# Kernel optimization log

Measured on AMD Instinct MI355X. Metric: run time of the kernel, lower is better.

## Reference

```python
import jax, jax.numpy as jnp
import numpy as np

N_HEAD = 16

def setup_inputs() -> dict:
    key = jax.random.key(0)
    ks = jax.random.split(key, 9)
    H = 2048
    def w(k, shape, scale=0.02):
        return jax.random.normal(k, shape, dtype=jnp.float32) * scale
    return {
        'h':  jax.random.normal(ks[0], (4, 2048, H), dtype=jnp.float32),
        'Wq': w(ks[1], (H, H)), 'bq': w(ks[2], (H,)),
        'Wk': w(ks[3], (H, H)), 'bk': w(ks[4], (H,)),
        'Wv': w(ks[5], (H, H)), 'bv': w(ks[6], (H,)),
        'Wo': w(ks[7], (H, H)), 'bo': w(ks[8], (H,)),
    }

def reference(h, Wq, bq, Wk, bk, Wv, bv, Wo, bo):
    B, S, H = h.shape
    nh = N_HEAD
    hd = H // nh
    # QKV projections (torch Linear: x @ W.T + b)
    q = (h @ Wq.T + bq).reshape(B, S, nh, hd)
    k = (h @ Wk.T + bk).reshape(B, S, nh, hd)
    v = (h @ Wv.T + bv).reshape(B, S, nh, hd)
    scale = 1.0 / jnp.sqrt(jnp.float32(hd))
    # causal attention scores [B, nh, S, S]
    scores = jnp.einsum('bqhd,bkhd->bhqk', q, k) * scale
    causal = jnp.tril(jnp.ones((S, S), dtype=bool))
    scores = jnp.where(causal, scores, jnp.finfo(scores.dtype).min)
    attn = jax.nn.softmax(scores, axis=-1)
    o = jnp.einsum('bhqk,bkhd->bqhd', attn, v).reshape(B, S, H)
    return o @ Wo.T + bo
```

## Files before the change

### kernel.cpp

```cpp
#include <hip/hip_runtime.h>
#include <hip/hip_bf16.h>
#include <math.h>


using bf16x8 = __attribute__((ext_vector_type(8))) __bf16;
using f32x4  = __attribute__((ext_vector_type(4))) float;
using s16x8  = __attribute__((ext_vector_type(8))) short;

#define MFMA16(a, b, c) __builtin_amdgcn_mfma_f32_16x16x32_bf16((a), (b), (c), 0, 0, 0)

__device__ __forceinline__ unsigned short f2bf(float f) {
  unsigned u = __float_as_uint(f);
  u += 0x7FFFu + ((u >> 16) & 1u);
  return (unsigned short)(u >> 16);
}

__device__ __forceinline__ void gload16(const void* g, void* l) {
  __builtin_amdgcn_global_load_lds((const __attribute__((address_space(1))) void*)g,
                                   (__attribute__((address_space(3))) void*)l,
                                   16, 0, 0);
}

__global__ void cvt_kernel(const float* __restrict__ in, unsigned short* __restrict__ out, int n4) {
  int i = blockIdx.x * 256 + threadIdx.x;
  if (i >= n4) return;
  float4 v = ((const float4*)in)[i];
  ushort4 o;
  o.x = f2bf(v.x); o.y = f2bf(v.y); o.z = f2bf(v.z); o.w = f2bf(v.w);
  ((ushort4*)out)[i] = o;
}

__global__ void cvtW_kernel(const float* __restrict__ s0, const float* __restrict__ s1,
                            const float* __restrict__ s2, const float* __restrict__ s3,
                            unsigned short* __restrict__ dqkv, unsigned short* __restrict__ dwo) {
  int i = blockIdx.x * 256 + threadIdx.x;
  int which = i >> 20;
  const float* s = (which == 0) ? s0 : (which == 1) ? s1 : (which == 2) ? s2 : s3;
  unsigned short* d = (which < 3) ? dqkv + which * 4194304 : dwo;
  int j = i & 1048575;
  float4 v = ((const float4*)s)[j];
  ushort4 o;
  o.x = f2bf(v.x); o.y = f2bf(v.y); o.z = f2bf(v.z); o.w = f2bf(v.w);
  ((ushort4*)d)[j] = o;
}


#define GEMM_PRE()                                                             \
  const int tid = threadIdx.x;                                                 \
  const int wave = tid >> 6, lane = tid & 63;                                  \
  const int lo = lane & 15, hi = lane >> 4;                                    \
  const int wr = wave >> 2, wc = wave & 3;                                     \
  const int r4 = lane >> 2, s4 = lane & 3;                                     \
  const int scol = ((s4 ^ ((r4 >> 1) & 3)) << 3);                              \
  const unsigned short* aS[2]; const unsigned short* bS[2];                    \
  _Pragma("unroll")                                                            \
  for (int j = 0; j < 2; ++j) {                                                \
    aS[j] = A + (size_t)(m0 + (wave * 2 + j) * 16 + r4) * 2048 + scol;         \
    bS[j] = W + (size_t)(n0 + (wave * 2 + j) * 16 + r4) * 2048 + scol;         \
  }                                                                            \
  f32x4 acc[8][4] = {};

#define STAGE2(BUF, J)                                                         \
  do {                                                                         \
    gload16(aS[J], &lA[BUF][(wave * 2 + (J)) * 512]);                          \
    gload16(bS[J], &lB[BUF][(wave * 2 + (J)) * 512]);                          \
    aS[J] += 32; bS[J] += 32;                                                  \
  } while (0)

#define LDA4_(dst, MH, BUF)                                                    \
  do {                                                                         \
    _Pragma("unroll")                                                          \
    for (int im = 0; im < 4; ++im)                                             \
      dst[im] = *(const bf16x8*)&lA[BUF][(wr * 128 + (MH)*64 + im * 16 + lo) * 32 + \
                                         ((hi ^ ((lo >> 1) & 3)) << 3)];       \
  } while (0)

#define LDB4_(dst, BUF)                                                        \
  do {                                                                         \
    _Pragma("unroll")                                                          \
    for (int ni = 0; ni < 4; ++ni)                                             \
      dst[ni] = *(const bf16x8*)&lB[BUF][(wc * 64 + ni * 16 + lo) * 32 +       \
                                         ((hi ^ ((lo >> 1) & 3)) << 3)];       \
  } while (0)

#define MF16(MH, aF, bF)                                                       \
  do {                                                                         \
    __builtin_amdgcn_s_setprio(1);                                             \
    _Pragma("unroll")                                                          \
    for (int im = 0; im < 4; ++im)                                             \
      _Pragma("unroll")                                                        \
      for (int ni = 0; ni < 4; ++ni)                                           \
        acc[(MH)*4 + im][ni] = MFMA16(aF[im], bF[ni], acc[(MH)*4 + im][ni]);   \
    __builtin_amdgcn_s_setprio(0);                                             \
  } while (0)

#define BAR __builtin_amdgcn_s_barrier()
#define VMC(N) asm volatile("s_waitcnt vmcnt(" #N ")" ::: "memory")

#define TILE(RBUF, SBUF, COND, VN)                                             \
  do {                                                                         \
    bf16x8 aF[4], aG[4], bF[4];                                                \
    LDA4_(aF, 0, RBUF); LDB4_(bF, RBUF);                                       \
    if (COND) STAGE2(SBUF, 0);                                                 \
    BAR; MF16(0, aF, bF); BAR;                                                 \
    LDA4_(aG, 1, RBUF);                                                        \
    if (COND) STAGE2(SBUF, 1);                                                 \
    BAR; MF16(1, aG, bF); VMC(VN); BAR;                                        \
  } while (0)

#define GEMM_MAIN()                                                            \
  STAGE2(0, 0); STAGE2(0, 1); STAGE2(1, 0); STAGE2(1, 1);                      \
  STAGE2(2, 0); STAGE2(2, 1);                                                  \
  VMC(8); BAR;                                                                 \
  for (int u = 0; u < 15; ++u) {                                               \
    TILE(0, 3, true, 8); TILE(1, 0, true, 8);                                  \
    TILE(2, 1, true, 8); TILE(3, 2, true, 8);                                  \
  }                                                                            \
  TILE(0, 3, true, 8); TILE(1, 0, false, 4);                                   \
  TILE(2, 1, false, 0); TILE(3, 2, false, 0);

__global__ __launch_bounds__(512, 2)
void gemm_qkv(const unsigned short* __restrict__ A,
              const unsigned short* __restrict__ W,
              const float* __restrict__ bq, const float* __restrict__ bk,
              const float* __restrict__ bv,
              unsigned short* __restrict__ Q, unsigned short* __restrict__ Kq,
              unsigned short* __restrict__ V) {
  __shared__ unsigned short lA[4][256 * 32];
  __shared__ unsigned short lB[4][256 * 32];
  const int bid = blockIdx.x;
  const int sid = (bid & 7) * 96 + (bid >> 3);
  const int bm = sid / 24, bn = sid % 24;
  const int m0 = bm * 256, n0 = bn * 256;
  GEMM_PRE();
  GEMM_MAIN();

  const int which = n0 >> 11;
  const float* bias = (which == 0) ? bq : (which == 1) ? bk : bv;
  unsigned short* dst = (which == 0) ? Q : (which == 1) ? Kq : V;
#pragma unroll
  for (int mi = 0; mi < 8; mi++)
#pragma unroll
    for (int ni = 0; ni < 4; ni++) {
      int n_g = n0 + wc * 64 + ni * 16 + lo;
      int n2 = n_g & 2047;
      int head = n2 >> 7, d = n2 & 127;
      float bb = bias[n2];
#pragma unroll
      for (int i = 0; i < 4; i++) {
        int m = m0 + wr * 128 + mi * 16 + hi * 4 + i;
        int b = m >> 11, s = m & 2047;
        dst[(((size_t)b * 16 + head) * 2048 + s) * 128 + d] = f2bf(acc[mi][ni][i] + bb);
      }
    }
}

__global__ __launch_bounds__(512, 2)
void gemm_out(const unsigned short* __restrict__ A,
              const unsigned short* __restrict__ W,
              const float* __restrict__ bo, float* __restrict__ out) {
  __shared__ unsigned short lA[4][256 * 32];
  __shared__ unsigned short lB[4][256 * 32];
  const int bid = blockIdx.x;
  const int sid = (bid & 7) * 32 + (bid >> 3);
  const int bm = sid >> 3, bn = sid & 7;
  const int m0 = bm * 256, n0 = bn * 256;
  GEMM_PRE();
  GEMM_MAIN();

#pragma unroll
  for (int mi = 0; mi < 8; mi++)
#pragma unroll
    for (int ni = 0; ni < 4; ni++) {
      int n_g = n0 + wc * 64 + ni * 16 + lo;
      float bb = bo[n_g];
#pragma unroll
      for (int i = 0; i < 4; i++) {
        int m = m0 + wr * 128 + mi * 16 + hi * 4 + i;
        out[(size_t)m * 2048 + n_g] = acc[mi][ni][i] + bb;
      }
    }
}

__global__ __launch_bounds__(256, 2)
void attn_kernel(const unsigned short* __restrict__ Qb,
                 const unsigned short* __restrict__ Kb,
                 const unsigned short* __restrict__ Vb,
                 unsigned short* __restrict__ Ob) {
  __shared__ unsigned short lK[2][64 * 128];
  __shared__ unsigned short lVt[144 * 72];
  __shared__ unsigned short lP[4][32 * 72];

  const int tid = threadIdx.x;
  const int wave = tid >> 6, lane = tid & 63;
  const int lo = lane & 15, hi = lane >> 4;
  const int bh = blockIdx.x & 63;
  const int qt = 15 - (blockIdx.x >> 6);
  const int q0 = qt * 128 + wave * 32;
  const size_t base = (size_t)bh * 2048 * 128;
  const float SCL = 0.08838834764831845f * 1.4426950408889634f;
  const float THR = 11.5416f;

#pragma unroll
  for (int x = tid; x < 1024; x += 256)
    lVt[(128 + (x >> 6)) * 72 + (x & 63)] = 0x3F80;

  bf16x8 aq[2][4];
#pragma unroll
  for (int mi = 0; mi < 2; mi++)
#pragma unroll
    for (int dk = 0; dk < 4; dk++)
      aq[mi][dk] = *(const bf16x8*)&Qb[base + (size_t)(q0 + mi * 16 + lo) * 128 + dk * 32 + hi * 8];

  f32x4 acc[2][9] = {};
  float mrun[2][4];
#pragma unroll
  for (int a = 0; a < 2; a++)
#pragma unroll
    for (int b = 0; b < 4; b++) mrun[a][b] = -INFINITY;

  const int ktn = qt * 2 + 2;
  const int qmax_w = q0 + 31;
  const int rr = tid & 31, c0v = (tid >> 5) * 8;

#define STAGEK(KT2, BUF)                                                       \
  do {                                                                         \
    _Pragma("unroll")                                                          \
    for (int j = 0; j < 4; j++) {                                              \
      int lrow = j * 16 + wave * 4 + hi;                                       \
      int srccol = (lo * 16) ^ ((lrow & 7) << 4);                              \
      gload16(Kb + base + (size_t)((KT2) * 64 + lrow) * 128 + (srccol >> 1),   \
              &lK[BUF][(j * 16 + wave * 4) * 128]);                            \
    }                                                                          \
  } while (0)

  STAGEK(0, 0);

  for (int kt = 0; kt < ktn; kt++) {
    const unsigned short* vp0 = Vb + base + (size_t)(kt * 64 + 2 * rr) * 128 + c0v;
    s16x8 v00 = *(const s16x8*)vp0;
    s16x8 v01 = *(const s16x8*)(vp0 + 128);
    s16x8 v10 = *(const s16x8*)(vp0 + 64);
    s16x8 v11 = *(const s16x8*)(vp0 + 192);
    if (kt + 1 < ktn) { STAGEK(kt + 1, (kt + 1) & 1); VMC(8); }
    else { VMC(0); }
    BAR;

    const bool docomp = (kt * 64 <= qmax_w);
    if (docomp) {
      const unsigned short* lKc = &lK[kt & 1][0];
      f32x4 sc[2][4] = {};
      __builtin_amdgcn_s_setprio(1);
#pragma unroll
      for (int ni = 0; ni < 4; ni++)
#pragma unroll
        for (int dk = 0; dk < 4; dk++) {
          int row = ni * 16 + lo;
          int col = (dk * 32 + hi * 8) ^ ((row & 7) << 3);
          bf16x8 bk_ = *(const bf16x8*)&lKc[row * 128 + col];
          sc[0][ni] = MFMA16(aq[0][dk], bk_, sc[0][ni]);
          sc[1][ni] = MFMA16(aq[1][dk], bk_, sc[1][ni]);
        }
      __builtin_amdgcn_s_setprio(0);
      float tm[2][4];
      bool cond = true;
#pragma unroll
      for (int mi = 0; mi < 2; mi++)
#pragma unroll
        for (int i = 0; i < 4; i++) {
          int qrow = q0 + mi * 16 + hi * 4 + i;
          float mx = -INFINITY;
#pragma unroll
          for (int ni = 0; ni < 4; ni++) {
            int kc = kt * 64 + ni * 16 + lo;
            float s = sc[mi][ni][i] * SCL;
            if (kc > qrow) s = -INFINITY;
            sc[mi][ni][i] = s;
            mx = fmaxf(mx, s);
          }
          tm[mi][i] = mx;
          cond = cond && (mx <= mrun[mi][i] + THR);
        }
      if (!__all((int)cond)) {
#pragma unroll
        for (int mi = 0; mi < 2; mi++)
#pragma unroll
          for (int i = 0; i < 4; i++) {
            float mt = tm[mi][i];
            mt = fmaxf(mt, __shfl_xor(mt, 1));
            mt = fmaxf(mt, __shfl_xor(mt, 2));
            mt = fmaxf(mt, __shfl_xor(mt, 4));
            mt = fmaxf(mt, __shfl_xor(mt, 8));
            float mo = mrun[mi][i];
            float mn = fmaxf(mo, mt);
            float alpha = exp2f(mo - mn);
            mrun[mi][i] = mn;
#pragma unroll
            for (int ni = 0; ni < 9; ni++) acc[mi][ni][i] *= alpha;
          }
      }
      unsigned short* lPw = &lP[wave][0];
#pragma unroll
      for (int mi = 0; mi < 2; mi++)
#pragma unroll
        for (int i = 0; i < 4; i++) {
          float m = mrun[mi][i];
          int prow = mi * 16 + hi * 4 + i;
#pragma unroll
          for (int ni = 0; ni < 4; ni++)
            lPw[prow * 72 + ni * 16 + lo] = f2bf(exp2f(sc[mi][ni][i] - m));
        }
    }

#pragma unroll
    for (int j = 0; j < 8; j++) {
      *(ushort2*)&lVt[(c0v + j) * 72 + 2 * rr] =
          make_ushort2((unsigned short)v00[j], (unsigned short)v01[j]);
      *(ushort2*)&lVt[(c0v + 64 + j) * 72 + 2 * rr] =
          make_ushort2((unsigned short)v10[j], (unsigned short)v11[j]);
    }
    asm volatile("s_waitcnt lgkmcnt(0)" ::: "memory");
    BAR;

    if (docomp) {
      unsigned short* lPw = &lP[wave][0];
      bf16x8 ap[2][2];
#pragma unroll
      for (int mi = 0; mi < 2; mi++)
#pragma unroll
        for (int k2 = 0; k2 < 2; k2++)
          ap[mi][k2] = *(const bf16x8*)&lPw[(mi * 16 + lo) * 72 + k2 * 32 + hi * 8];
      __builtin_amdgcn_s_setprio(1);
#pragma unroll
      for (int ni = 0; ni < 9; ni++)
#pragma unroll
        for (int k2 = 0; k2 < 2; k2++) {
          bf16x8 bv_ = *(const bf16x8*)&lVt[(ni * 16 + lo) * 72 + k2 * 32 + hi * 8];
          acc[0][ni] = MFMA16(ap[0][k2], bv_, acc[0][ni]);
          acc[1][ni] = MFMA16(ap[1][k2], bv_, acc[1][ni]);
        }
      __builtin_amdgcn_s_setprio(0);
    }
  }

  const int b = bh >> 4, hh = bh & 15;
#pragma unroll
  for (int mi = 0; mi < 2; mi++)
#pragma unroll
    for (int i = 0; i < 4; i++) {
      float inv = 1.0f / acc[mi][8][i];
      int s = q0 + mi * 16 + hi * 4 + i;
      size_t rowbase = ((size_t)b * 2048 + s) * 2048 + hh * 128 + lo;
#pragma unroll
      for (int ni = 0; ni < 8; ni++)
        Ob[rowbase + ni * 16] = f2bf(acc[mi][ni][i] * inv);
    }
}

extern "C" void kernel_launch(void* const* d_in, const int* in_sizes, int n_in,
                              void* d_out, int out_size, void* d_ws, size_t ws_size,
                              hipStream_t stream) {
  const float* h  = (const float*)d_in[0];
  const float* Wq = (const float*)d_in[1];
  const float* bq = (const float*)d_in[2];
  const float* Wk = (const float*)d_in[3];
  const float* bk = (const float*)d_in[4];
  const float* Wv = (const float*)d_in[5];
  const float* bv = (const float*)d_in[6];
  const float* Wo = (const float*)d_in[7];
  const float* bo = (const float*)d_in[8];
  float* out = (float*)d_out;

  char* ws = (char*)d_ws;
  unsigned short* h_bf  = (unsigned short*)(ws + 0);
  unsigned short* Qb    = (unsigned short*)(ws + 33554432);
  unsigned short* Kb    = (unsigned short*)(ws + 67108864);
  unsigned short* Vb    = (unsigned short*)(ws + 100663296);
  unsigned short* Wqkv  = (unsigned short*)(ws + 134217728);
  unsigned short* Wo_bf = (unsigned short*)(ws + 159383552);
  unsigned short* Ob    = h_bf;

  cvt_kernel<<<16384, 256, 0, stream>>>(h, h_bf, 4194304);
  cvtW_kernel<<<16384, 256, 0, stream>>>(Wq, Wk, Wv, Wo, Wqkv, Wo_bf);

  gemm_qkv<<<dim3(768), dim3(512), 0, stream>>>(h_bf, Wqkv, bq, bk, bv, Qb, Kb, Vb);

  attn_kernel<<<dim3(1024), dim3(256), 0, stream>>>(Qb, Kb, Vb, Ob);

  gemm_out<<<dim3(256), dim3(512), 0, stream>>>(Ob, Wo_bf, bo, out);
}
```

Measured before the change: 431.8 us.

## Shrink GEMM tiles to 128x256 with triple-buffered LDS and higher occupancy

The QKV and output GEMMs switch from 256x256 to 128x256 block tiles. The LDS pipeline changes from 4 stages to 3 stages, and launch bounds now request 4 blocks per CU instead of 2. The grid size doubles, which mainly helps the out-projection: it previously launched only 256 blocks. The cost is less operand reuse per block, more total global/L2 traffic, and fewer MFMAs per barrier.

```diff
diff --git a/kernel.cpp b/kernel.cpp
--- a/kernel.cpp
+++ b/kernel.cpp
@@ -52,45 +52,42 @@
   const int wr = wave >> 2, wc = wave & 3;                                     \
   const int r4 = lane >> 2, s4 = lane & 3;                                     \
   const int scol = ((s4 ^ ((r4 >> 1) & 3)) << 3);                              \
-  const unsigned short* aS[2]; const unsigned short* bS[2];                    \
-  _Pragma("unroll")                                                            \
-  for (int j = 0; j < 2; ++j) {                                                \
-    aS[j] = A + (size_t)(m0 + (wave * 2 + j) * 16 + r4) * 2048 + scol;         \
-    bS[j] = W + (size_t)(n0 + (wave * 2 + j) * 16 + r4) * 2048 + scol;         \
-  }                                                                            \
-  f32x4 acc[8][4] = {};
-
-#define STAGE2(BUF, J)                                                         \
-  do {                                                                         \
-    gload16(aS[J], &lA[BUF][(wave * 2 + (J)) * 512]);                          \
-    gload16(bS[J], &lB[BUF][(wave * 2 + (J)) * 512]);                          \
-    aS[J] += 32; bS[J] += 32;                                                  \
-  } while (0)
-
-#define LDA4_(dst, MH, BUF)                                                    \
+  const int swz = ((hi ^ ((lo >> 1) & 3)) << 3);                               \
+  const unsigned short* aS; const unsigned short* bS[2];                       \
+  aS = A + (size_t)(m0 + wave * 16 + r4) * 2048 + scol;                        \
+  bS[0] = W + (size_t)(n0 + (wave * 2 + 0) * 16 + r4) * 2048 + scol;           \
+  bS[1] = W + (size_t)(n0 + (wave * 2 + 1) * 16 + r4) * 2048 + scol;           \
+  f32x4 acc[4][4] = {};
+
+#define STAGE3(BUF)                                                            \
+  do {                                                                         \
+    gload16(aS, &lA[BUF][wave * 512]); aS += 32;                               \
+    gload16(bS[0], &lB[BUF][(wave * 2 + 0) * 512]); bS[0] += 32;               \
+    gload16(bS[1], &lB[BUF][(wave * 2 + 1) * 512]); bS[1] += 32;               \
+  } while (0)
+
+#define LDA4_(dst, BUF)                                                        \
   do {                                                                         \
     _Pragma("unroll")                                                          \
     for (int im = 0; im < 4; ++im)                                             \
-      dst[im] = *(const bf16x8*)&lA[BUF][(wr * 128 + (MH)*64 + im * 16 + lo) * 32 + \
-                                         ((hi ^ ((lo >> 1) & 3)) << 3)];       \
+      dst[im] = *(const bf16x8*)&lA[BUF][(wr * 64 + im * 16 + lo) * 32 + swz]; \
   } while (0)
 
 #define LDB4_(dst, BUF)                                                        \
   do {                                                                         \
     _Pragma("unroll")                                                          \
     for (int ni = 0; ni < 4; ++ni)                                             \
-      dst[ni] = *(const bf16x8*)&lB[BUF][(wc * 64 + ni * 16 + lo) * 32 +       \
-                                         ((hi ^ ((lo >> 1) & 3)) << 3)];       \
-  } while (0)
-
-#define MF16(MH, aF, bF)                                                       \
+      dst[ni] = *(const bf16x8*)&lB[BUF][(wc * 64 + ni * 16 + lo) * 32 + swz]; \
+  } while (0)
+
+#define MF16(aF, bF)                                                           \
   do {                                                                         \
     __builtin_amdgcn_s_setprio(1);                                             \
     _Pragma("unroll")                                                          \
     for (int im = 0; im < 4; ++im)                                             \
       _Pragma("unroll")                                                        \
       for (int ni = 0; ni < 4; ++ni)                                           \
-        acc[(MH)*4 + im][ni] = MFMA16(aF[im], bF[ni], acc[(MH)*4 + im][ni]);   \
+        acc[im][ni] = MFMA16(aF[im], bF[ni], acc[im][ni]);                     \
     __builtin_amdgcn_s_setprio(0);                                             \
   } while (0)
 
@@ -99,39 +96,34 @@
 
 #define TILE(RBUF, SBUF, COND, VN)                                             \
   do {                                                                         \
-    bf16x8 aF[4], aG[4], bF[4];                                                \
-    LDA4_(aF, 0, RBUF); LDB4_(bF, RBUF);                                       \
-    if (COND) STAGE2(SBUF, 0);                                                 \
-    BAR; MF16(0, aF, bF); BAR;                                                 \
-    LDA4_(aG, 1, RBUF);                                                        \
-    if (COND) STAGE2(SBUF, 1);                                                 \
-    BAR; MF16(1, aG, bF); VMC(VN); BAR;                                        \
+    bf16x8 aF[4], bF[4];                                                       \
+    LDA4_(aF, RBUF); LDB4_(bF, RBUF);                                          \
+    if (COND) STAGE3(SBUF);                                                    \
+    BAR; MF16(aF, bF); VMC(VN); BAR;                                           \
   } while (0)
 
 #define GEMM_MAIN()                                                            \
-  STAGE2(0, 0); STAGE2(0, 1); STAGE2(1, 0); STAGE2(1, 1);                      \
-  STAGE2(2, 0); STAGE2(2, 1);                                                  \
-  VMC(8); BAR;                                                                 \
-  for (int u = 0; u < 15; ++u) {                                               \
-    TILE(0, 3, true, 8); TILE(1, 0, true, 8);                                  \
-    TILE(2, 1, true, 8); TILE(3, 2, true, 8);                                  \
+  STAGE3(0); STAGE3(1);                                                        \
+  VMC(3); BAR;                                                                 \
+  for (int u = 0; u < 20; ++u) {                                               \
+    TILE(0, 2, true, 3); TILE(1, 0, true, 3); TILE(2, 1, true, 3);             \
   }                                                                            \
-  TILE(0, 3, true, 8); TILE(1, 0, false, 4);                                   \
-  TILE(2, 1, false, 0); TILE(3, 2, false, 0);
-
-__global__ __launch_bounds__(512, 2)
+  TILE(0, 2, true, 3); TILE(1, 0, true, 3);                                    \
+  TILE(2, 1, false, 0); TILE(0, 0, false, 0);
+
+__global__ __launch_bounds__(512, 4)
 void gemm_qkv(const unsigned short* __restrict__ A,
               const unsigned short* __restrict__ W,
               const float* __restrict__ bq, const float* __restrict__ bk,
               const float* __restrict__ bv,
               unsigned short* __restrict__ Q, unsigned short* __restrict__ Kq,
               unsigned short* __restrict__ V) {
-  __shared__ unsigned short lA[4][256 * 32];
-  __shared__ unsigned short lB[4][256 * 32];
+  __shared__ unsigned short lA[3][128 * 32];
+  __shared__ unsigned short lB[3][256 * 32];
   const int bid = blockIdx.x;
-  const int sid = (bid & 7) * 96 + (bid >> 3);
+  const int sid = (bid & 7) * 192 + (bid >> 3);
   const int bm = sid / 24, bn = sid % 24;
-  const int m0 = bm * 256, n0 = bn * 256;
+  const int m0 = bm * 128, n0 = bn * 256;
   GEMM_PRE();
   GEMM_MAIN();
 
@@ -139,7 +131,7 @@
   const float* bias = (which == 0) ? bq : (which == 1) ? bk : bv;
   unsigned short* dst = (which == 0) ? Q : (which == 1) ? Kq : V;
 #pragma unroll
-  for (int mi = 0; mi < 8; mi++)
+  for (int mi = 0; mi < 4; mi++)
 #pragma unroll
     for (int ni = 0; ni < 4; ni++) {
       int n_g = n0 + wc * 64 + ni * 16 + lo;
@@ -148,35 +140,35 @@
       float bb = bias[n2];
 #pragma unroll
       for (int i = 0; i < 4; i++) {
-        int m = m0 + wr * 128 + mi * 16 + hi * 4 + i;
+        int m = m0 + wr * 64 + mi * 16 + hi * 4 + i;
         int b = m >> 11, s = m & 2047;
         dst[(((size_t)b * 16 + head) * 2048 + s) * 128 + d] = f2bf(acc[mi][ni][i] + bb);
       }
     }
 }
 
-__global__ __launch_bounds__(512, 2)
+__global__ __launch_bounds__(512, 4)
 void gemm_out(const unsigned short* __restrict__ A,
               const unsigned short* __restrict__ W,
               const float* __restrict__ bo, float* __restrict__ out) {
-  __shared__ unsigned short lA[4][256 * 32];
-  __shared__ unsigned short lB[4][256 * 32];
+  __shared__ unsigned short lA[3][128 * 32];
+  __shared__ unsigned short lB[3][256 * 32];
   const int bid = blockIdx.x;
-  const int sid = (bid & 7) * 32 + (bid >> 3);
+  const int sid = (bid & 7) * 64 + (bid >> 3);
   const int bm = sid >> 3, bn = sid & 7;
-  const int m0 = bm * 256, n0 = bn * 256;
+  const int m0 = bm * 128, n0 = bn * 256;
   GEMM_PRE();
   GEMM_MAIN();
 
 #pragma unroll
-  for (int mi = 0; mi < 8; mi++)
+  for (int mi = 0; mi < 4; mi++)
 #pragma unroll
     for (int ni = 0; ni < 4; ni++) {
       int n_g = n0 + wc * 64 + ni * 16 + lo;
       float bb = bo[n_g];
 #pragma unroll
       for (int i = 0; i < 4; i++) {
-        int m = m0 + wr * 128 + mi * 16 + hi * 4 + i;
+        int m = m0 + wr * 64 + mi * 16 + hi * 4 + i;
         out[(size_t)m * 2048 + n_g] = acc[mi][ni][i] + bb;
       }
     }
@@ -383,9 +375,9 @@
   cvt_kernel<<<16384, 256, 0, stream>>>(h, h_bf, 4194304);
   cvtW_kernel<<<16384, 256, 0, stream>>>(Wq, Wk, Wv, Wo, Wqkv, Wo_bf);
 
-  gemm_qkv<<<dim3(768), dim3(512), 0, stream>>>(h_bf, Wqkv, bq, bk, bv, Qb, Kb, Vb);
+  gemm_qkv<<<dim3(1536), dim3(512), 0, stream>>>(h_bf, Wqkv, bq, bk, bv, Qb, Kb, Vb);
 
   attn_kernel<<<dim3(1024), dim3(256), 0, stream>>>(Qb, Kb, Vb, Ob);
 
-  gemm_out<<<dim3(256), dim3(512), 0, stream>>>(Ob, Wo_bf, bo, out);
-}
+  gemm_out<<<dim3(512), dim3(512), 0, stream>>>(Ob, Wo_bf, bo, out);
+}
```

Result: slower. 470.9 us (+9.1%).

## Software-pipeline LDS fragment loads across GEMM k-tiles with double-buffered registers

Applied to the files above, without the earlier changes.

Restructures the GEMM main loop so the LDS fragment reads for the next half-tile and the next k-tile are issued before the MFMAs of the current one, using ping-pong register buffers for the B fragments. Explicit lgkmcnt waits and sched_barriers are added, and the vmcnt thresholds are adjusted to match the new staging order. The goal is to hide LDS read latency behind MFMA work. In exchange it uses more VGPRs, which may pressure occupancy at 512 threads with 2 blocks, and the barrier and waitcnt ordering carries a risk of subtle races.

```diff
diff --git a/kernel.cpp b/kernel.cpp
--- a/kernel.cpp
+++ b/kernel.cpp
@@ -58,7 +58,8 @@
     aS[j] = A + (size_t)(m0 + (wave * 2 + j) * 16 + r4) * 2048 + scol;         \
     bS[j] = W + (size_t)(n0 + (wave * 2 + j) * 16 + r4) * 2048 + scol;         \
   }                                                                            \
-  f32x4 acc[8][4] = {};
+  f32x4 acc[8][4] = {};                                                        \
+  bf16x8 aA_[4], aB_[4], bX[4], bY[4];
 
 #define STAGE2(BUF, J)                                                         \
   do {                                                                         \
@@ -96,28 +97,53 @@
 
 #define BAR __builtin_amdgcn_s_barrier()
 #define VMC(N) asm volatile("s_waitcnt vmcnt(" #N ")" ::: "memory")
-
-#define TILE(RBUF, SBUF, COND, VN)                                             \
-  do {                                                                         \
-    bf16x8 aF[4], aG[4], bF[4];                                                \
-    LDA4_(aF, 0, RBUF); LDB4_(bF, RBUF);                                       \
-    if (COND) STAGE2(SBUF, 0);                                                 \
-    BAR; MF16(0, aF, bF); BAR;                                                 \
-    LDA4_(aG, 1, RBUF);                                                        \
-    if (COND) STAGE2(SBUF, 1);                                                 \
-    BAR; MF16(1, aG, bF); VMC(VN); BAR;                                        \
+#define LGKM0                                                                  \
+  do {                                                                         \
+    asm volatile("s_waitcnt lgkmcnt(0)" ::: "memory");                         \
+    __builtin_amdgcn_sched_barrier(0);                                         \
+  } while (0)
+
+#define TILE2(RBUF, NBUF, SBUF, bC, bN, C1, C2, VN)                            \
+  do {                                                                         \
+    BAR; LGKM0;                                                                \
+    LDA4_(aB_, 1, RBUF);                                                       \
+    if (C1) STAGE2(SBUF, 0);                                                   \
+    MF16(0, aA_, bC);                                                          \
+    BAR;                                                                       \
+    VMC(VN); BAR; LGKM0;                                                       \
+    LDA4_(aA_, 0, NBUF);                                                       \
+    LDB4_(bN, NBUF);                                                           \
+    if (C2) STAGE2(SBUF, 1);                                                   \
+    MF16(1, aB_, bC);                                                          \
+    BAR;                                                                       \
+  } while (0)
+
+#define TILE_LAST(RBUF, bC)                                                    \
+  do {                                                                         \
+    BAR; LGKM0;                                                                \
+    LDA4_(aB_, 1, RBUF);                                                       \
+    MF16(0, aA_, bC);                                                          \
+    BAR;                                                                       \
+    BAR; LGKM0;                                                                \
+    MF16(1, aB_, bC);                                                          \
+    BAR;                                                                       \
   } while (0)
 
 #define GEMM_MAIN()                                                            \
   STAGE2(0, 0); STAGE2(0, 1); STAGE2(1, 0); STAGE2(1, 1);                      \
   STAGE2(2, 0); STAGE2(2, 1);                                                  \
-  VMC(8); BAR;                                                                 \
+  VMC(6); BAR;                                                                 \
+  LDA4_(aA_, 0, 0); LDB4_(bX, 0);                                              \
   for (int u = 0; u < 15; ++u) {                                               \
-    TILE(0, 3, true, 8); TILE(1, 0, true, 8);                                  \
-    TILE(2, 1, true, 8); TILE(3, 2, true, 8);                                  \
+    TILE2(0, 1, 3, bX, bY, true, true, 6);                                     \
+    TILE2(1, 2, 0, bY, bX, true, true, 6);                                     \
+    TILE2(2, 3, 1, bX, bY, true, true, 6);                                     \
+    TILE2(3, 0, 2, bY, bX, true, true, 6);                                     \
   }                                                                            \
-  TILE(0, 3, true, 8); TILE(1, 0, false, 4);                                   \
-  TILE(2, 1, false, 0); TILE(3, 2, false, 0);
+  TILE2(0, 1, 3, bX, bY, true, true, 6);                                       \
+  TILE2(1, 2, 0, bY, bX, false, false, 4);                                     \
+  TILE2(2, 3, 1, bX, bY, false, false, 0);                                     \
+  TILE_LAST(3, bY);
 
 __global__ __launch_bounds__(512, 2)
 void gemm_qkv(const unsigned short* __restrict__ A,
```

New measurement: 438.2 us. About the same (+1.5%).
